# Kernel optimization log

Measured on AMD Instinct MI355X. Metric: run time of the kernel, lower is better.

The kernel has to match this reference:

```python
import jax, jax.numpy as jnp
import numpy as np

INPUT_NC = 512
N_HEADS = 16
D_KEY = 64
SCALE = D_KEY ** 0.5


def setup_inputs() -> dict:
    key = jax.random.key(0)
    k1, k2, k3, k4, k5, k6 = jax.random.split(key, 6)
    bs, d_seq = 8, 1024
    v = jax.random.normal(k1, (bs, d_seq, INPUT_NC), dtype=jnp.float32)
    # key-padding mask, True = masked out; broadcast over heads and query dim
    pad_mask = jax.random.bernoulli(k2, 0.1, (bs, 1, 1, d_seq))
    # fc1: input_nc -> 2*n_heads*d_key (fused K,Q projection)
    W1 = jax.random.normal(k3, (INPUT_NC, 2 * N_HEADS * D_KEY), dtype=jnp.float32) * (1.0 / np.sqrt(INPUT_NC))
    b1 = jax.random.normal(k4, (2 * N_HEADS * D_KEY,), dtype=jnp.float32) * 0.01
    # fc2: n_heads*input_nc -> input_nc
    W2 = jax.random.normal(k5, (N_HEADS * INPUT_NC, INPUT_NC), dtype=jnp.float32) * (1.0 / np.sqrt(N_HEADS * INPUT_NC))
    b2 = jax.random.normal(k6, (INPUT_NC,), dtype=jnp.float32) * 0.01
    return {"v": v, "pad_mask": pad_mask, "W1": W1, "b1": b1, "W2": W2, "b2": b2}


def reference(v, pad_mask, W1, b1, W2, b2):
    bs, d_seq, nc = v.shape
    # fused KQ projection: [bs, S, 2*H*dk] -> [bs, H, S, 2*dk]
    kq = (v @ W1 + b1).reshape(bs, d_seq, N_HEADS, 2 * D_KEY).transpose(0, 2, 1, 3)
    k, q = kq[..., :D_KEY], kq[..., D_KEY:]  # chunk: k first, q second
    attn = jnp.einsum('bhqd,bhkd->bhqk', q, k) / SCALE
    attn = jnp.where(pad_mask, jnp.float32(-1000.0), attn)
    attn = jax.nn.softmax(attn, axis=3)
    # AV with unprojected v broadcast across heads: [bs, H, S, nc]
    out = jnp.einsum('bhqk,bkc->bhqc', attn, v)
    out = out.transpose(0, 2, 1, 3).reshape(bs, d_seq, N_HEADS * nc)
    out = out @ W2 + b2
    return (out, attn)
```

## Files before the change

### kernel.cpp

```cpp
#include <hip/hip_runtime.h>


typedef __attribute__((ext_vector_type(8))) short bf16x8;
typedef __attribute__((ext_vector_type(4))) float f32x4;
typedef __attribute__((ext_vector_type(4))) unsigned short u16x4;

__device__ __forceinline__ unsigned short f2bf(float f) {
  unsigned u = __builtin_bit_cast(unsigned, f);
  u += 0x7FFFu + ((u >> 16) & 1u);
  return (unsigned short)(u >> 16);
}
__device__ __forceinline__ float bf2f(unsigned short u) {
  return __builtin_bit_cast(float, (unsigned)u << 16);
}

__device__ __forceinline__ void gload_lds16(const unsigned short* g, unsigned short* l) {
  __builtin_amdgcn_global_load_lds(
      (const __attribute__((address_space(1))) unsigned int*)(g),
      (__attribute__((address_space(3))) unsigned int*)(l), 16, 0, 0);
}

#define WAITV(N) do { asm volatile("s_waitcnt vmcnt(" #N ")" ::: "memory"); \
                      __builtin_amdgcn_sched_barrier(0); } while (0)
#define BAR()    do { __builtin_amdgcn_s_barrier(); \
                      __builtin_amdgcn_sched_barrier(0); } while (0)


__global__ void transpose_cvt_kernel(const float* __restrict__ in,
                                     unsigned short* __restrict__ out,
                                     int R, int C) {
  __shared__ float tile[32][33];
  int c0 = blockIdx.x * 32, r0 = blockIdx.y * 32;
  int tx = threadIdx.x & 31, ty = threadIdx.x >> 5;
#pragma unroll
  for (int i = ty; i < 32; i += 8)
    tile[i][tx] = in[(size_t)(r0 + i) * C + (c0 + tx)];
  __syncthreads();
#pragma unroll
  for (int i = ty; i < 32; i += 8)
    out[(size_t)(c0 + i) * R + (r0 + tx)] = f2bf(tile[tx][i]);
}

__global__ void prep_v_kernel(const float* __restrict__ v,
                              unsigned short* __restrict__ vbf,
                              unsigned short* __restrict__ vt) {
  __shared__ float tile[32][33];
  int c0 = blockIdx.x * 32, r0 = blockIdx.y * 32;
  int tx = threadIdx.x & 31, ty = threadIdx.x >> 5;
#pragma unroll
  for (int i = ty; i < 32; i += 8) {
    float val = v[(size_t)(r0 + i) * 512 + (c0 + tx)];
    tile[i][tx] = val;
    vbf[(size_t)(r0 + i) * 512 + (c0 + tx)] = f2bf(val);
  }
  __syncthreads();
#pragma unroll
  for (int i = ty; i < 32; i += 8)
    vt[(size_t)(c0 + i) * 8192 + (r0 + tx)] = f2bf(tile[tx][i]);
}

__launch_bounds__(256)
__global__ void gemm1_kernel(const unsigned short* __restrict__ vbf,
                             const unsigned short* __restrict__ w1t,
                             const float* __restrict__ b1,
                             unsigned short* __restrict__ q_ws,
                             unsigned short* __restrict__ k_ws) {
  const int m0 = blockIdx.y * 128, n0 = blockIdx.x * 128;
  const int w = threadIdx.x >> 6, l = threadIdx.x & 63;
  const int wr = w >> 1, wc = w & 1, lr = l & 15, lg = l >> 4;
  f32x4 acc[4][4];
#pragma unroll
  for (int mi = 0; mi < 4; ++mi)
#pragma unroll
    for (int ni = 0; ni < 4; ++ni) acc[mi][ni] = (f32x4){0.f, 0.f, 0.f, 0.f};

  for (int k0 = 0; k0 < 512; k0 += 32) {
    bf16x8 a[4], bb[4];
#pragma unroll
    for (int mi = 0; mi < 4; ++mi)
      a[mi] = *reinterpret_cast<const bf16x8*>(
          vbf + (size_t)(m0 + wr * 64 + mi * 16 + lr) * 512 + k0 + lg * 8);
#pragma unroll
    for (int ni = 0; ni < 4; ++ni)
      bb[ni] = *reinterpret_cast<const bf16x8*>(
          w1t + (size_t)(n0 + wc * 64 + ni * 16 + lr) * 512 + k0 + lg * 8);
#pragma unroll
    for (int mi = 0; mi < 4; ++mi)
#pragma unroll
      for (int ni = 0; ni < 4; ++ni)
        acc[mi][ni] = __builtin_amdgcn_mfma_f32_16x16x32_bf16(a[mi], bb[ni], acc[mi][ni], 0, 0, 0);
  }
#pragma unroll
  for (int mi = 0; mi < 4; ++mi)
#pragma unroll
    for (int ni = 0; ni < 4; ++ni) {
      int col = n0 + wc * 64 + ni * 16 + lr;
      int h = col >> 7, j = col & 127;
      float bias = b1[col];
#pragma unroll
      for (int r = 0; r < 4; ++r) {
        int row = m0 + wr * 64 + mi * 16 + lg * 4 + r;
        int bb_ = row >> 10, s = row & 1023;
        unsigned short bv = f2bf(acc[mi][ni][r] + bias);
        size_t base = ((size_t)(bb_ * 16 + h) << 16) + (size_t)s * 64;
        if (j < 64) k_ws[base + j] = bv;
        else        q_ws[base + j - 64] = bv;
      }
    }
}

__launch_bounds__(512)
__global__ void scores_kernel(const unsigned short* __restrict__ q_ws,
                              const unsigned short* __restrict__ k_ws,
                              const int* __restrict__ pad,
                              float* __restrict__ attn_out,
                              unsigned short* __restrict__ eb,
                              float* __restrict__ linv_ws) {
  const int wg = (blockIdx.x & 7) * 512 + (blockIdx.x >> 3);
  const int qt = wg & 31, h = (wg >> 5) & 15, b = wg >> 9;
  const int bh = b * 16 + h, q0 = qt * 32;
  const int w = threadIdx.x >> 6, l = threadIdx.x & 63;
  const int lr = l & 15, lg = l >> 4;

  __shared__ unsigned short E_lds[32][1032];
  __shared__ float lw[8][32];
  __shared__ float linv_s[32];

  const unsigned short* qb = q_ws + ((size_t)bh << 16);
  const unsigned short* kb = k_ws + ((size_t)bh << 16);
  const int* pmb = pad + b * 1024;

  bf16x8 a_q[2][2];
#pragma unroll
  for (int mf = 0; mf < 2; ++mf)
#pragma unroll
    for (int ks = 0; ks < 2; ++ks)
      a_q[mf][ks] = *reinterpret_cast<const bf16x8*>(
          qb + (size_t)(q0 + mf * 16 + lr) * 64 + ks * 32 + lg * 8);

  float l_run[2][4];
#pragma unroll
  for (int mf = 0; mf < 2; ++mf)
#pragma unroll
    for (int r = 0; r < 4; ++r) l_run[mf][r] = 0.f;

#pragma unroll
  for (int sub = 0; sub < 2; ++sub) {
    const int c0 = w * 128 + sub * 64;
    f32x4 s[2][4];
#pragma unroll
    for (int mf = 0; mf < 2; ++mf)
#pragma unroll
      for (int nf = 0; nf < 4; ++nf) s[mf][nf] = (f32x4){0.f, 0.f, 0.f, 0.f};
#pragma unroll
    for (int ks = 0; ks < 2; ++ks) {
      bf16x8 bk[4];
#pragma unroll
      for (int nf = 0; nf < 4; ++nf)
        bk[nf] = *reinterpret_cast<const bf16x8*>(
            kb + (size_t)(c0 + nf * 16 + lr) * 64 + ks * 32 + lg * 8);
#pragma unroll
      for (int mf = 0; mf < 2; ++mf)
#pragma unroll
        for (int nf = 0; nf < 4; ++nf)
          s[mf][nf] = __builtin_amdgcn_mfma_f32_16x16x32_bf16(a_q[mf][ks], bk[nf], s[mf][nf], 0, 0, 0);
    }
    int msk[4];
#pragma unroll
    for (int nf = 0; nf < 4; ++nf) msk[nf] = pmb[c0 + nf * 16 + lr];
#pragma unroll
    for (int mf = 0; mf < 2; ++mf)
#pragma unroll
      for (int nf = 0; nf < 4; ++nf)
#pragma unroll
        for (int r = 0; r < 4; ++r) {
          float e = msk[nf] ? 0.f : __expf(s[mf][nf][r] * 0.125f);
          l_run[mf][r] += e;
          E_lds[mf * 16 + lg * 4 + r][c0 + nf * 16 + lr] = f2bf(e);
        }
  }

#pragma unroll
  for (int mf = 0; mf < 2; ++mf)
#pragma unroll
    for (int r = 0; r < 4; ++r) {
      float v = l_run[mf][r];
      v += __shfl_xor(v, 1); v += __shfl_xor(v, 2);
      v += __shfl_xor(v, 4); v += __shfl_xor(v, 8);
      if (lr == 0) lw[w][mf * 16 + lg * 4 + r] = v;
    }
  __syncthreads();
  if (threadIdx.x < 32) {
    float s = 0.f;
#pragma unroll
    for (int ww = 0; ww < 8; ++ww) s += lw[ww][threadIdx.x];
    float li = 1.f / s;
    linv_s[threadIdx.x] = li;
    linv_ws[(size_t)bh * 1024 + q0 + threadIdx.x] = li;
  }
  __syncthreads();

  {
    const int row = threadIdx.x >> 4;
    const int cb = threadIdx.x & 15;
    const float sc = linv_s[row];
    float* rowp = attn_out + ((size_t)bh << 20) + (size_t)(q0 + row) * 1024;
    unsigned short* ebrow = eb + ((size_t)bh << 20) + (size_t)(q0 + row) * 1024;
#pragma unroll
    for (int i = 0; i < 8; ++i) {
      int c8 = cb * 8 + i * 128;
      bf16x8 ev = *reinterpret_cast<const bf16x8*>(&E_lds[row][c8]);
      f32x4 o0, o1;
#pragma unroll
      for (int j = 0; j < 4; ++j) o0[j] = bf2f((unsigned short)ev[j]) * sc;
#pragma unroll
      for (int j = 0; j < 4; ++j) o1[j] = bf2f((unsigned short)ev[4 + j]) * sc;
      *reinterpret_cast<f32x4*>(rowp + c8) = o0;
      *reinterpret_cast<f32x4*>(rowp + c8 + 4) = o1;
      *reinterpret_cast<bf16x8*>(ebrow + c8) = ev;
    }
  }
}

__launch_bounds__(256)
__global__ void pv_kernel(const unsigned short* __restrict__ eb,
                          const unsigned short* __restrict__ vt,
                          const float* __restrict__ linv_ws,
                          unsigned short* __restrict__ o_ws) {
  const int wg = (blockIdx.x & 7) * 512 + (blockIdx.x >> 3);
  const int nt = wg & 3, mt = (wg >> 2) & 7, bh = wg >> 5;
  const int b = bh >> 4, h = bh & 15;
  const int m0 = mt * 128, n0 = nt * 128;

  __shared__ unsigned short Asm[3][128 * 32];
  __shared__ unsigned short Bsm[3][128 * 32];
  const int w = threadIdx.x >> 6, l = threadIdx.x & 63;
  const int wr = w >> 1, wc = w & 1, lr = l & 15, lg = l >> 4;

  f32x4 acc[4][4];
#pragma unroll
  for (int mi = 0; mi < 4; ++mi)
#pragma unroll
    for (int ni = 0; ni < 4; ++ni) acc[mi][ni] = (f32x4){0.f, 0.f, 0.f, 0.f};

  const int srow = threadIdx.x >> 2;
  const int scol = (((threadIdx.x & 3) ^ (srow & 3)) * 8);
  const unsigned short* gA0 = eb + ((size_t)bh << 20) + (size_t)(m0 + srow) * 1024 + scol;
  const unsigned short* gA1 = gA0 + (size_t)64 * 1024;
  const unsigned short* gB0 = vt + (size_t)(n0 + srow) * 8192 + (size_t)b * 1024 + scol;
  const unsigned short* gB1 = gB0 + (size_t)64 * 8192;
  const int ldsoff = w * 512;
  const int sl = (lg ^ (lr & 3)) * 8;

  auto STAGE = [&](int buf, int kt) {
    int k0 = kt * 32;
    gload_lds16(gA0 + k0, &Asm[buf][ldsoff]);
    gload_lds16(gA1 + k0, &Asm[buf][64 * 32 + ldsoff]);
    gload_lds16(gB0 + k0, &Bsm[buf][ldsoff]);
    gload_lds16(gB1 + k0, &Bsm[buf][64 * 32 + ldsoff]);
  };
  auto COMPUTE = [&](int buf) {
    bf16x8 a[4], bb[4];
#pragma unroll
    for (int mi = 0; mi < 4; ++mi)
      a[mi] = *reinterpret_cast<const bf16x8*>(&Asm[buf][(wr * 64 + mi * 16 + lr) * 32 + sl]);
#pragma unroll
    for (int ni = 0; ni < 4; ++ni)
      bb[ni] = *reinterpret_cast<const bf16x8*>(&Bsm[buf][(wc * 64 + ni * 16 + lr) * 32 + sl]);
    __builtin_amdgcn_s_setprio(1);
#pragma unroll
    for (int mi = 0; mi < 4; ++mi)
#pragma unroll
      for (int ni = 0; ni < 4; ++ni)
        acc[mi][ni] = __builtin_amdgcn_mfma_f32_16x16x32_bf16(a[mi], bb[ni], acc[mi][ni], 0, 0, 0);
    __builtin_amdgcn_s_setprio(0);
  };

  STAGE(0, 0); STAGE(1, 1); STAGE(2, 2);
  int cur = 0;
  for (int kt = 0; kt < 29; ++kt) {
    WAITV(8);
    BAR();
    COMPUTE(cur);
    BAR();
    STAGE(cur, kt + 3);
    cur = (cur == 2) ? 0 : cur + 1;
  }
  WAITV(8); BAR(); COMPUTE(cur); cur = (cur == 2) ? 0 : cur + 1;
  WAITV(4); BAR(); COMPUTE(cur); cur = (cur == 2) ? 0 : cur + 1;
  WAITV(0); BAR(); COMPUTE(cur);

  float linv_r[4][4];
  {
    const float* lrow = linv_ws + (size_t)bh * 1024 + m0 + wr * 64 + lg * 4;
#pragma unroll
    for (int mi = 0; mi < 4; ++mi)
#pragma unroll
      for (int r = 0; r < 4; ++r) linv_r[mi][r] = lrow[mi * 16 + r];
  }

#pragma unroll
  for (int mi = 0; mi < 4; ++mi)
#pragma unroll
    for (int ni = 0; ni < 4; ++ni)
#pragma unroll
      for (int r = 0; r < 4; ++r) {
        int row = m0 + wr * 64 + mi * 16 + lg * 4 + r;
        int col = n0 + wc * 64 + ni * 16 + lr;
        o_ws[(size_t)(b * 1024 + row) * 8192 + h * 512 + col] =
            f2bf(acc[mi][ni][r] * linv_r[mi][r]);
      }
}

__launch_bounds__(256)
__global__ void gemm2_kernel(const unsigned short* __restrict__ o_ws,
                             const unsigned short* __restrict__ w2t,
                             const float* __restrict__ b2,
                             float* __restrict__ y) {
  const int wg = (blockIdx.x & 7) * 64 + (blockIdx.x >> 3);
  const int nt = wg & 3, mt = wg >> 2;
  const int m0 = mt * 64, n0 = nt * 128;

  __shared__ unsigned short As[3][64 * 32];
  __shared__ unsigned short Bs[3][128 * 32];
  const int w = threadIdx.x >> 6, l = threadIdx.x & 63;
  const int wr = w >> 1, wc = w & 1, lr = l & 15, lg = l >> 4;

  f32x4 acc[2][4];
#pragma unroll
  for (int mi = 0; mi < 2; ++mi)
#pragma unroll
    for (int ni = 0; ni < 4; ++ni) acc[mi][ni] = (f32x4){0.f, 0.f, 0.f, 0.f};

  const int srow = threadIdx.x >> 2;
  const int scol = (((threadIdx.x & 3) ^ (srow & 3)) * 8);
  const unsigned short* gA  = o_ws + (size_t)(m0 + srow) * 8192 + scol;
  const unsigned short* gB0 = w2t + (size_t)(n0 + srow) * 8192 + scol;
  const unsigned short* gB1 = gB0 + (size_t)64 * 8192;
  const int ldsoff = w * 512;
  const int sl = (lg ^ (lr & 3)) * 8;

  auto STAGE = [&](int buf, int kt) {
    int k0 = kt * 32;
    gload_lds16(gA + k0, &As[buf][ldsoff]);
    gload_lds16(gB0 + k0, &Bs[buf][ldsoff]);
    gload_lds16(gB1 + k0, &Bs[buf][64 * 32 + ldsoff]);
  };

  auto COMPUTE = [&](int buf) {
    bf16x8 a[2], bb[4];
#pragma unroll
    for (int mi = 0; mi < 2; ++mi)
      a[mi] = *reinterpret_cast<const bf16x8*>(&As[buf][(wr * 32 + mi * 16 + lr) * 32 + sl]);
#pragma unroll
    for (int ni = 0; ni < 4; ++ni)
      bb[ni] = *reinterpret_cast<const bf16x8*>(&Bs[buf][(wc * 64 + ni * 16 + lr) * 32 + sl]);
    __builtin_amdgcn_s_setprio(1);
#pragma unroll
    for (int mi = 0; mi < 2; ++mi)
#pragma unroll
      for (int ni = 0; ni < 4; ++ni)
        acc[mi][ni] = __builtin_amdgcn_mfma_f32_16x16x32_bf16(a[mi], bb[ni], acc[mi][ni], 0, 0, 0);
    __builtin_amdgcn_s_setprio(0);
  };

  STAGE(0, 0); STAGE(1, 1); STAGE(2, 2);
  int cur = 0;
  for (int kt = 0; kt < 253; ++kt) {
    WAITV(6);
    BAR();
    COMPUTE(cur);
    BAR();
    STAGE(cur, kt + 3);
    cur = (cur == 2) ? 0 : cur + 1;
  }
  WAITV(6); BAR(); COMPUTE(cur); cur = (cur == 2) ? 0 : cur + 1;
  WAITV(3); BAR(); COMPUTE(cur); cur = (cur == 2) ? 0 : cur + 1;
  WAITV(0); BAR(); COMPUTE(cur);

#pragma unroll
  for (int mi = 0; mi < 2; ++mi)
#pragma unroll
    for (int ni = 0; ni < 4; ++ni) {
      int col = n0 + wc * 64 + ni * 16 + lr;
      float bias = b2[col];
#pragma unroll
      for (int r = 0; r < 4; ++r)
        y[(size_t)(m0 + wr * 32 + mi * 16 + lg * 4 + r) * 512 + col] = acc[mi][ni][r] + bias;
    }
}

extern "C" void kernel_launch(void* const* d_in, const int* in_sizes, int n_in,
                              void* d_out, int out_size, void* d_ws, size_t ws_size,
                              hipStream_t stream) {
  const float* v   = (const float*)d_in[0];
  const int*   pad = (const int*)d_in[1];
  const float* W1  = (const float*)d_in[2];
  const float* b1  = (const float*)d_in[3];
  const float* W2  = (const float*)d_in[4];
  const float* b2  = (const float*)d_in[5];
  float* out  = (float*)d_out;
  float* attn = out + (size_t)8 * 1024 * 512;

  char* ws = (char*)d_ws;
  unsigned short* w1t  = (unsigned short*)(ws);
  unsigned short* w2t  = (unsigned short*)(ws + 2097152);
  unsigned short* vt   = (unsigned short*)(ws + 10485760);
  unsigned short* vbf  = (unsigned short*)(ws + 18874368);
  unsigned short* q_ws = (unsigned short*)(ws + 27262976);
  unsigned short* k_ws = (unsigned short*)(ws + 44040192);
  unsigned short* o_ws = (unsigned short*)(ws + 60817408);
  unsigned short* eb   = (unsigned short*)(ws + 195035136);
  float*          linv = (float*)(ws + 463470592);

  transpose_cvt_kernel<<<dim3(64, 16), 256, 0, stream>>>(W1, w1t, 512, 2048);
  transpose_cvt_kernel<<<dim3(16, 256), 256, 0, stream>>>(W2, w2t, 8192, 512);
  prep_v_kernel<<<dim3(16, 256), 256, 0, stream>>>(v, vbf, vt);
  gemm1_kernel<<<dim3(16, 64), 256, 0, stream>>>(vbf, w1t, b1, q_ws, k_ws);
  scores_kernel<<<4096, 512, 0, stream>>>(q_ws, k_ws, pad, attn, eb, linv);
  pv_kernel<<<4096, 256, 0, stream>>>(eb, vt, linv, o_ws);
  gemm2_kernel<<<512, 256, 0, stream>>>(o_ws, w2t, b2, out);
}
```

Baseline: 673.2 us.

## Use 4-stage double-step pipelines in GEMMs and early bf16 E writeback

Both pv and gemm2 kernels move from a 3-buffer, one-k-step-per-barrier loop to 4 LDS buffers that compute two k-tiles per barrier pair. This halves the barriers per k-tile and allows deeper prefetch. The attention kernel now writes the bf16 E tile to global right after the exp loop, before the row-sum reduction, so the stores overlap the reductions. It also swaps __syncthreads for explicit lgkmcnt waits plus barriers. The cost is more LDS per block, which may lower occupancy, and a fixed tail that assumes particular k-tile counts.

```diff
diff --git a/kernel.cpp b/kernel.cpp
--- a/kernel.cpp
+++ b/kernel.cpp
@@ -23,6 +23,10 @@
 #define WAITV(N) do { asm volatile("s_waitcnt vmcnt(" #N ")" ::: "memory"); \
                       __builtin_amdgcn_sched_barrier(0); } while (0)
 #define BAR()    do { __builtin_amdgcn_s_barrier(); \
+                      __builtin_amdgcn_sched_barrier(0); } while (0)
+#define LBAR()   do { asm volatile("s_waitcnt lgkmcnt(0)" ::: "memory"); \
+                      __builtin_amdgcn_sched_barrier(0); \
+                      __builtin_amdgcn_s_barrier(); \
                       __builtin_amdgcn_sched_barrier(0); } while (0)
 
 
@@ -180,6 +184,20 @@
         }
   }
 
+  {
+    asm volatile("s_waitcnt lgkmcnt(0)" ::: "memory");
+    __builtin_amdgcn_sched_barrier(0);
+    const int rl = l >> 4;
+    const int cb8 = (l & 15) * 8;
+    unsigned short* ebw = eb + ((size_t)bh << 20) + (size_t)q0 * 1024 + w * 128 + cb8;
+#pragma unroll
+    for (int it = 0; it < 8; ++it) {
+      int row = it * 4 + rl;
+      *reinterpret_cast<bf16x8*>(ebw + (size_t)row * 1024) =
+          *reinterpret_cast<const bf16x8*>(&E_lds[row][w * 128 + cb8]);
+    }
+  }
+
 #pragma unroll
   for (int mf = 0; mf < 2; ++mf)
 #pragma unroll
@@ -189,7 +207,7 @@
       v += __shfl_xor(v, 4); v += __shfl_xor(v, 8);
       if (lr == 0) lw[w][mf * 16 + lg * 4 + r] = v;
     }
-  __syncthreads();
+  LBAR();
   if (threadIdx.x < 32) {
     float s = 0.f;
 #pragma unroll
@@ -198,14 +216,13 @@
     linv_s[threadIdx.x] = li;
     linv_ws[(size_t)bh * 1024 + q0 + threadIdx.x] = li;
   }
-  __syncthreads();
+  LBAR();
 
   {
     const int row = threadIdx.x >> 4;
     const int cb = threadIdx.x & 15;
     const float sc = linv_s[row];
     float* rowp = attn_out + ((size_t)bh << 20) + (size_t)(q0 + row) * 1024;
-    unsigned short* ebrow = eb + ((size_t)bh << 20) + (size_t)(q0 + row) * 1024;
 #pragma unroll
     for (int i = 0; i < 8; ++i) {
       int c8 = cb * 8 + i * 128;
@@ -217,7 +234,6 @@
       for (int j = 0; j < 4; ++j) o1[j] = bf2f((unsigned short)ev[4 + j]) * sc;
       *reinterpret_cast<f32x4*>(rowp + c8) = o0;
       *reinterpret_cast<f32x4*>(rowp + c8 + 4) = o1;
-      *reinterpret_cast<bf16x8*>(ebrow + c8) = ev;
     }
   }
 }
@@ -232,8 +248,8 @@
   const int b = bh >> 4, h = bh & 15;
   const int m0 = mt * 128, n0 = nt * 128;
 
-  __shared__ unsigned short Asm[3][128 * 32];
-  __shared__ unsigned short Bsm[3][128 * 32];
+  __shared__ unsigned short Asm[4][128 * 32];
+  __shared__ unsigned short Bsm[4][128 * 32];
   const int w = threadIdx.x >> 6, l = threadIdx.x & 63;
   const int wr = w >> 1, wc = w & 1, lr = l & 15, lg = l >> 4;
 
@@ -276,19 +292,19 @@
     __builtin_amdgcn_s_setprio(0);
   };
 
-  STAGE(0, 0); STAGE(1, 1); STAGE(2, 2);
-  int cur = 0;
-  for (int kt = 0; kt < 29; ++kt) {
+  STAGE(0, 0); STAGE(1, 1); STAGE(2, 2); STAGE(3, 3);
+  for (int i = 0; i < 14; ++i) {
+    const int b0 = (2 * i) & 3, b1 = (2 * i + 1) & 3;
     WAITV(8);
     BAR();
-    COMPUTE(cur);
+    COMPUTE(b0);
+    COMPUTE(b1);
     BAR();
-    STAGE(cur, kt + 3);
-    cur = (cur == 2) ? 0 : cur + 1;
-  }
-  WAITV(8); BAR(); COMPUTE(cur); cur = (cur == 2) ? 0 : cur + 1;
-  WAITV(4); BAR(); COMPUTE(cur); cur = (cur == 2) ? 0 : cur + 1;
-  WAITV(0); BAR(); COMPUTE(cur);
+    STAGE(b0, 2 * i + 4);
+    STAGE(b1, 2 * i + 5);
+  }
+  WAITV(8); BAR(); COMPUTE(0); COMPUTE(1);
+  WAITV(0); BAR(); COMPUTE(2); COMPUTE(3);
 
   float linv_r[4][4];
   {
@@ -321,8 +337,8 @@
   const int nt = wg & 3, mt = wg >> 2;
   const int m0 = mt * 64, n0 = nt * 128;
 
-  __shared__ unsigned short As[3][64 * 32];
-  __shared__ unsigned short Bs[3][128 * 32];
+  __shared__ unsigned short As[4][64 * 32];
+  __shared__ unsigned short Bs[4][128 * 32];
   const int w = threadIdx.x >> 6, l = threadIdx.x & 63;
   const int wr = w >> 1, wc = w & 1, lr = l & 15, lg = l >> 4;
 
@@ -364,19 +380,19 @@
     __builtin_amdgcn_s_setprio(0);
   };
 
-  STAGE(0, 0); STAGE(1, 1); STAGE(2, 2);
-  int cur = 0;
-  for (int kt = 0; kt < 253; ++kt) {
+  STAGE(0, 0); STAGE(1, 1); STAGE(2, 2); STAGE(3, 3);
+  for (int i = 0; i < 126; ++i) {
+    const int b0 = (2 * i) & 3, b1 = (2 * i + 1) & 3;
     WAITV(6);
     BAR();
-    COMPUTE(cur);
+    COMPUTE(b0);
+    COMPUTE(b1);
     BAR();
-    STAGE(cur, kt + 3);
-    cur = (cur == 2) ? 0 : cur + 1;
-  }
-  WAITV(6); BAR(); COMPUTE(cur); cur = (cur == 2) ? 0 : cur + 1;
-  WAITV(3); BAR(); COMPUTE(cur); cur = (cur == 2) ? 0 : cur + 1;
-  WAITV(0); BAR(); COMPUTE(cur);
+    STAGE(b0, 2 * i + 4);
+    STAGE(b1, 2 * i + 5);
+  }
+  WAITV(6); BAR(); COMPUTE(0); COMPUTE(1);
+  WAITV(0); BAR(); COMPUTE(2); COMPUTE(3);
 
 #pragma unroll
   for (int mi = 0; mi < 2; ++mi)
```

After: 678.1 us. No clear change (+0.7%).
